# Performance work log

Hardware: AMD Instinct MI355X
Metric: run time of the kernel (lower is better)

The kernel has to match this reference:

```python
import jax, jax.numpy as jnp
import numpy as np
import math

D_MODEL = 768
D_INNER = 1536   # expand_factor=2
D_STATE = 16
DT_RANK = 48     # ceil(768/16)
D_CONV = 4
B, L = 2, 1024


def setup_inputs() -> dict:
    key = jax.random.key(0)
    ks = jax.random.split(key, 16)
    rn = lambda k, shape, s: jax.random.normal(k, shape, jnp.float32) * s
    dt_std = DT_RANK ** -0.5
    # dt bias init: softplus-inverse of dt in [dt_min, dt_max]
    dt = jnp.exp(jax.random.uniform(ks[6], (D_INNER,)) * (math.log(0.1) - math.log(0.001)) + math.log(0.001))
    dt = jnp.clip(dt, 1e-4, None)
    inv_dt = dt + jnp.log(-jnp.expm1(-dt))
    A_init = jnp.log(jnp.tile(jnp.arange(1, D_STATE + 1, dtype=jnp.float32), (D_INNER, 1)))
    return {
        "x": jax.random.normal(ks[0], (B, L, D_MODEL), jnp.float32),
        "in_proj_w": rn(ks[1], (2 * D_INNER, D_MODEL), D_MODEL ** -0.5),
        "conv_w": rn(ks[2], (D_INNER, D_CONV), D_CONV ** -0.5),
        "conv_bias": rn(ks[3], (D_INNER,), 0.02),
        "x_proj_w": rn(ks[4], (DT_RANK + 2 * D_STATE, D_INNER), D_INNER ** -0.5),
        "dt_proj_w": jax.random.uniform(ks[5], (D_INNER, DT_RANK), jnp.float32, -dt_std, dt_std),
        "dt_proj_b": inv_dt,
        "A_log": A_init,
        "D_param": jnp.ones((D_INNER,), jnp.float32),
        "out_proj_w": rn(ks[7], (D_MODEL, D_INNER), D_INNER ** -0.5),
        "A_b_log": A_init,
        "x_proj_b_w": rn(ks[8], (DT_RANK + 2 * D_STATE, D_INNER), D_INNER ** -0.5),
        "dt_proj_b_w": jax.random.uniform(ks[9], (D_INNER, DT_RANK), jnp.float32, -dt_std, dt_std),
        "dt_proj_b_b": inv_dt,
        "D_b": jnp.ones((D_INNER,), jnp.float32),
    }


def _ssm_dir(xs, A_log, Dv, xpw, dtw, dtb):
    # xs: [B, L, ED]
    A = -jnp.exp(A_log)                                  # [ED, N]
    dbc = xs @ xpw.T                                     # [B, L, dt_rank + 2N]
    delta = jax.nn.softplus(dbc[..., :DT_RANK] @ dtw.T + dtb)   # [B, L, ED]
    Bm = dbc[..., DT_RANK:DT_RANK + D_STATE]             # [B, L, N]
    Cm = dbc[..., DT_RANK + D_STATE:]                    # [B, L, N]
    dA = jnp.exp(delta[..., None] * A)                   # [B, L, ED, N]
    dBx = (delta * xs)[..., None] * Bm[:, :, None, :]    # [B, L, ED, N]

    def comb(e1, e2):
        a1, h1 = e1
        a2, h2 = e2
        return (a2 * a1, a2 * h1 + h2)

    _, hs = jax.lax.associative_scan(comb, (dA, dBx), axis=1)  # [B, L, ED, N]
    y = jnp.einsum('blen,bln->ble', hs, Cm)
    return y + Dv * xs


def reference(x, in_proj_w, conv_w, conv_bias, x_proj_w, dt_proj_w, dt_proj_b,
              A_log, D_param, out_proj_w, A_b_log, x_proj_b_w, dt_proj_b_w,
              dt_proj_b_b, D_b):
    xz = x @ in_proj_w.T                                 # [B, L, 2*ED]
    xs, z = xz[..., :D_INNER], xz[..., D_INNER:]
    # causal depthwise conv1d (torch pads both sides then slices [:L] == left pad)
    xt = jnp.transpose(xs, (0, 2, 1))                    # [B, ED, L]
    conv = jax.lax.conv_general_dilated(
        xt, conv_w[:, None, :], (1,), [(D_CONV - 1, 0)],
        feature_group_count=D_INNER,
        dimension_numbers=('NCW', 'OIW', 'NCW'))
    xs = jax.nn.silu(jnp.transpose(conv + conv_bias[:, None], (0, 2, 1)))
    y = _ssm_dir(xs, A_log, D_param, x_proj_w, dt_proj_w, dt_proj_b)
    yb = _ssm_dir(xs[:, ::-1], A_b_log, D_b, x_proj_b_w, dt_proj_b_w, dt_proj_b_b)
    y = y + yb[:, ::-1]
    return (y * jax.nn.silu(z)) @ out_proj_w.T
```

## Files before the change

kernel.cpp:

```cpp
#include <hip/hip_runtime.h>
#include <hip/hip_bf16.h>
#include <math.h>
#include <stdint.h>

#define D_MODEL 768
#define D_INNER 1536
#define D_STATE 16
#define DT_RANK 48
#define NB 2
#define LL 1024
#define MROWS (NB*LL)
#define NXZ (2*D_INNER)
#define NDBC 80

typedef __attribute__((ext_vector_type(8))) short short8;
typedef __attribute__((ext_vector_type(4))) float f32x4;

__device__ __forceinline__ float silu_f(float x) {
  return x / (1.0f + __expf(-x));
}
__device__ __forceinline__ float softplus_f(float x) {
  return (x >= 20.0f) ? x : log1pf(__expf(x));
}

__device__ __forceinline__ ushort f2bf(float x) {
  union { float f; uint32_t u; } v; v.f = x;
  return (ushort)((v.u + 0x7FFFu + ((v.u >> 16) & 1u)) >> 16);
}
__device__ __forceinline__ float bf2f(ushort h) {
  union { uint32_t u; float f; } v; v.u = ((uint32_t)h) << 16;
  return v.f;
}

__device__ __forceinline__ void g2l16(const void* g, void* l) {
  __builtin_amdgcn_global_load_lds(
      (const __attribute__((address_space(1))) uint32_t*)g,
      (__attribute__((address_space(3))) uint32_t*)l, 16, 0, 0);
}

__device__ __forceinline__ int swz(int row) {
  return (row ^ (row >> 2)) & 3;
}

__global__ __launch_bounds__(256)
void cvt_split_kernel(const float* __restrict__ in, ushort* __restrict__ hi,
                      ushort* __restrict__ lo, int n4) {
  int i = blockIdx.x * 256 + threadIdx.x;
  if (i >= n4) return;
  float4 v = *(const float4*)&in[i*4];
  ushort4 h, l;
  h.x = f2bf(v.x); l.x = f2bf(v.x - bf2f(h.x));
  h.y = f2bf(v.y); l.y = f2bf(v.y - bf2f(h.y));
  h.z = f2bf(v.z); l.z = f2bf(v.z - bf2f(h.z));
  h.w = f2bf(v.w); l.w = f2bf(v.w - bf2f(h.w));
  *(ushort4*)&hi[i*4] = h;
  *(ushort4*)&lo[i*4] = l;
}

template<int BM, int BN>
__global__ __launch_bounds__(256)
void gemm_mfma(const ushort* __restrict__ Ah, const ushort* __restrict__ Al,
               const ushort* __restrict__ Bh, const ushort* __restrict__ Bl,
               float* __restrict__ C, int M, int N, int K) {
  constexpr int MR = BM / 32;
  constexpr int NR = BN / 32;
  __shared__ __align__(16) ushort sAh[BM*32];
  __shared__ __align__(16) ushort sAl[BM*32];
  __shared__ __align__(16) ushort sBh[BN*32];
  __shared__ __align__(16) ushort sBl[BN*32];

  const int tid  = threadIdx.x;
  const int w    = tid >> 6;
  const int lane = tid & 63;
  const int wr   = w >> 1, wc = w & 1;
  const int bm   = blockIdx.x * BM, bn = blockIdx.y * BN;

  const int rA = lane >> 2;
  const int ps = lane & 3;
  const int kg = lane >> 4;
  const int fr = lane & 15;

  f32x4 acc[MR][NR];
  #pragma unroll
  for (int mi = 0; mi < MR; ++mi)
    #pragma unroll
    for (int ni = 0; ni < NR; ++ni) acc[mi][ni] = (f32x4){0.f,0.f,0.f,0.f};

  for (int k0 = 0; k0 < K; k0 += 32) {
    __syncthreads();
    #pragma unroll
    for (int q = 0; q < BM/64; ++q) {
      int row = q*64 + w*16 + rA;
      int kch = ps ^ swz(row);
      size_t go = (size_t)(bm + row)*K + k0 + kch*8;
      g2l16(Ah + go, (ushort*)sAh + (q*64 + w*16)*32);
      g2l16(Al + go, (ushort*)sAl + (q*64 + w*16)*32);
    }
    #pragma unroll
    for (int q = 0; q < BN/64; ++q) {
      int row = q*64 + w*16 + rA;
      int kch = ps ^ swz(row);
      size_t go = (size_t)(bn + row)*K + k0 + kch*8;
      g2l16(Bh + go, (ushort*)sBh + (q*64 + w*16)*32);
      g2l16(Bl + go, (ushort*)sBl + (q*64 + w*16)*32);
    }
    __syncthreads();

    short8 ah[MR], al[MR], bh[NR], bl[NR];
    #pragma unroll
    for (int mi = 0; mi < MR; ++mi) {
      int row  = wr*(BM/2) + mi*16 + fr;
      int slot = kg ^ swz(row);
      ah[mi] = *(const short8*)((const char*)sAh + row*64 + slot*16);
      al[mi] = *(const short8*)((const char*)sAl + row*64 + slot*16);
    }
    #pragma unroll
    for (int ni = 0; ni < NR; ++ni) {
      int row  = wc*(BN/2) + ni*16 + fr;
      int slot = kg ^ swz(row);
      bh[ni] = *(const short8*)((const char*)sBh + row*64 + slot*16);
      bl[ni] = *(const short8*)((const char*)sBl + row*64 + slot*16);
    }
    #pragma unroll
    for (int mi = 0; mi < MR; ++mi)
      #pragma unroll
      for (int ni = 0; ni < NR; ++ni) {
        acc[mi][ni] = __builtin_amdgcn_mfma_f32_16x16x32_bf16(ah[mi], bh[ni], acc[mi][ni], 0, 0, 0);
        acc[mi][ni] = __builtin_amdgcn_mfma_f32_16x16x32_bf16(ah[mi], bl[ni], acc[mi][ni], 0, 0, 0);
        acc[mi][ni] = __builtin_amdgcn_mfma_f32_16x16x32_bf16(al[mi], bh[ni], acc[mi][ni], 0, 0, 0);
      }
  }

  #pragma unroll
  for (int mi = 0; mi < MR; ++mi)
    #pragma unroll
    for (int ni = 0; ni < NR; ++ni) {
      #pragma unroll
      for (int r = 0; r < 4; ++r) {
        int m = bm + wr*(BM/2) + mi*16 + kg*4 + r;
        int n = bn + wc*(BN/2) + ni*16 + fr;
        C[(size_t)m*N + n] = acc[mi][ni][r];
      }
    }
}

__global__ __launch_bounds__(256)
void conv_silu_kernel(const float* __restrict__ xz, const float* __restrict__ cw,
                      const float* __restrict__ cb, float* __restrict__ xsc) {
  int idx = blockIdx.x * 256 + threadIdx.x;
  if (idx >= MROWS * D_INNER) return;
  int e   = idx % D_INNER;
  int row = idx / D_INNER;
  int l   = row % LL;
  const float* base = xz + (size_t)row * NXZ + e;
  float s = cb[e];
  #pragma unroll
  for (int j = 0; j < 4; ++j) {
    int dl = j - 3;
    if (l + dl >= 0) {
      int off = dl * NXZ;
      s = fmaf(cw[e*4 + j], base[off], s);
    }
  }
  xsc[idx] = silu_f(s);
}

__global__ __launch_bounds__(256)
void transpose_kernel(const float* __restrict__ in, float* __restrict__ outT) {
  __shared__ float T[64][65];
  const int m0 = blockIdx.x * 64;
  const int e0 = blockIdx.y * 64;
  const int cr = threadIdx.x >> 4;
  const int cc = (threadIdx.x & 15) * 4;
  for (int rr = cr; rr < 64; rr += 16) {
    float4 v = *(const float4*)&in[(size_t)(m0 + rr)*D_INNER + e0 + cc];
    T[rr][cc+0] = v.x; T[rr][cc+1] = v.y; T[rr][cc+2] = v.z; T[rr][cc+3] = v.w;
  }
  __syncthreads();
  for (int er = cr; er < 64; er += 16) {
    float4 v = make_float4(T[cc+0][er], T[cc+1][er], T[cc+2][er], T[cc+3][er]);
    *(float4*)&outT[(size_t)(e0 + er)*MROWS + m0 + cc] = v;
  }
}

__global__ __launch_bounds__(256)
void zero_kernel(float* __restrict__ p, int n) {
  int i = blockIdx.x * 256 + threadIdx.x;
  if (i < n) p[i] = 0.0f;
}

#define XP_BM 16
#define XP_KC 192
__global__ __launch_bounds__(256)
void xproj_kernel(const float* __restrict__ xsc, const float* __restrict__ wf,
                  const float* __restrict__ wb, float* __restrict__ dbcf,
                  float* __restrict__ dbcb) {
  __shared__ __align__(16) float As[16][XP_BM];
  __shared__ __align__(16) float Ws[16][164];
  const int m0    = blockIdx.x * XP_BM;
  const int kbase = blockIdx.y * XP_KC;
  const int tid = threadIdx.x;
  const int tx = tid & 31;
  const int ty = tid >> 5;
  float acc[2][5] = {};
  for (int k0 = kbase; k0 < kbase + XP_KC; k0 += 16) {
    __syncthreads();
    if (tid < 64) {
      int r = tid >> 2, c = (tid & 3) * 4;
      float4 v = *(const float4*)&xsc[(size_t)(m0 + r)*D_INNER + k0 + c];
      As[c+0][r] = v.x; As[c+1][r] = v.y; As[c+2][r] = v.z; As[c+3][r] = v.w;
    }
    for (int q = tid; q < 640; q += 256) {
      int r = q >> 2, c = (q & 3) * 4;
      const float* src = (r < 80) ? &wf[(size_t)r*D_INNER + k0 + c]
                                  : &wb[(size_t)(r-80)*D_INNER + k0 + c];
      float4 v = *(const float4*)src;
      Ws[c+0][r] = v.x; Ws[c+1][r] = v.y; Ws[c+2][r] = v.z; Ws[c+3][r] = v.w;
    }
    __syncthreads();
    #pragma unroll
    for (int kk = 0; kk < 16; ++kk) {
      float a0 = As[kk][ty*2 + 0];
      float a1 = As[kk][ty*2 + 1];
      #pragma unroll
      for (int j = 0; j < 5; ++j) {
        float w = Ws[kk][tx*5 + j];
        acc[0][j] = fmaf(a0, w, acc[0][j]);
        acc[1][j] = fmaf(a1, w, acc[1][j]);
      }
    }
  }
  #pragma unroll
  for (int i = 0; i < 2; ++i) {
    int m = m0 + ty*2 + i;
    #pragma unroll
    for (int j = 0; j < 5; ++j) {
      int n = tx*5 + j;
      float v = acc[i][j];
      if (n < 80) atomicAdd(&dbcf[(size_t)m*NDBC + n], v);
      else        atomicAdd(&dbcb[(size_t)m*NDBC + (n-80)], v);
    }
  }
}

__global__ __launch_bounds__(256)
void delta_kernel(const float* __restrict__ dbcf, const float* __restrict__ dbcb,
                  const float* __restrict__ dtwf, const float* __restrict__ dtwb,
                  const float* __restrict__ dtbf, const float* __restrict__ dtbb,
                  float* __restrict__ outf, float* __restrict__ outb) {
  const int dir = blockIdx.z;
  const float* dbc = dir ? dbcb : dbcf;
  const float* dtw = dir ? dtwb : dtwf;
  const float* dtb = dir ? dtbb : dtbf;
  float* out = dir ? outb : outf;
  __shared__ __align__(16) float As[48][36];
  __shared__ __align__(16) float Ws[48][132];
  __shared__ float T[128][33];
  const int m0 = blockIdx.x * 32;
  const int e0 = blockIdx.y * 128;
  const int tid = threadIdx.x;
  const int tx = tid & 31;
  const int ty = tid >> 5;
  for (int q = tid; q < 384; q += 256) {
    int r = q / 12, c = (q % 12) * 4;
    float4 v = *(const float4*)&dbc[(size_t)(m0 + r)*NDBC + c];
    As[c+0][r] = v.x; As[c+1][r] = v.y; As[c+2][r] = v.z; As[c+3][r] = v.w;
  }
  for (int q = tid; q < 1536; q += 256) {
    int r = q / 12, c = (q % 12) * 4;
    float4 v = *(const float4*)&dtw[(size_t)(e0 + r)*DT_RANK + c];
    Ws[c+0][r] = v.x; Ws[c+1][r] = v.y; Ws[c+2][r] = v.z; Ws[c+3][r] = v.w;
  }
  __syncthreads();
  float acc[4][4] = {};
  #pragma unroll
  for (int kk = 0; kk < 48; ++kk) {
    float4 a = *(const float4*)&As[kk][ty*4];
    float4 w = *(const float4*)&Ws[kk][tx*4];
    float av[4] = {a.x, a.y, a.z, a.w};
    float wv[4] = {w.x, w.y, w.z, w.w};
    #pragma unroll
    for (int i = 0; i < 4; ++i)
      #pragma unroll
      for (int j = 0; j < 4; ++j)
        acc[i][j] = fmaf(av[i], wv[j], acc[i][j]);
  }
  #pragma unroll
  for (int i = 0; i < 4; ++i)
    #pragma unroll
    for (int j = 0; j < 4; ++j)
      T[tx*4 + j][ty*4 + i] = softplus_f(acc[i][j] + dtb[e0 + tx*4 + j]);
  __syncthreads();
  {
    int r = tid >> 1, h = (tid & 1) * 16;
    float* dst = out + (size_t)(e0 + r)*MROWS + m0 + h;
    #pragma unroll
    for (int q = 0; q < 4; ++q) {
      float4 v = make_float4(T[r][h+q*4+0], T[r][h+q*4+1], T[r][h+q*4+2], T[r][h+q*4+3]);
      *(float4*)(dst + q*4) = v;
    }
  }
}

#define SC_C 16
#define SC_P 64
__global__ __launch_bounds__(1024)
void scan_kernel(const float* __restrict__ dltf, const float* __restrict__ dltb,
                 const float* __restrict__ dbcf, const float* __restrict__ dbcb,
                 const float* __restrict__ xst,
                 const float* __restrict__ Alogf, const float* __restrict__ Alogb,
                 float* __restrict__ yf, float* __restrict__ yb) {
  __shared__ float sA[SC_C][4][16];
  __shared__ float sH[SC_C][4][16];
  __shared__ float sI[SC_C][4][16];
  const int blk = blockIdx.x;
  const int dir = blk / 768;
  const int b   = (blk % 768) / 384;
  const int e0  = (blk % 384) * 4;
  const int tid = threadIdx.x;
  const int c   = tid >> 6;
  const int lane = tid & 63;
  const int es  = lane >> 4;
  const int n   = lane & 15;
  const int e   = e0 + es;

  const float* dlt  = dir ? dltb  : dltf;
  const float* dbc  = dir ? dbcb  : dbcf;
  const float* Alog = dir ? Alogb : Alogf;
  float* y          = dir ? yb    : yf;

  const float a2 = -__expf(Alog[e*D_STATE + n]) * 1.4426950408889634f;

  const int sg = dir ? -1 : 1;
  const int l0 = dir ? (LL - 1 - c*SC_P) : (c*SC_P);

  const float* dp0 = dlt + (size_t)e * MROWS + b * LL + l0;
  const float* xp0 = xst + (size_t)e * MROWS + b * LL + l0;
  const float* bp0 = dbc + ((size_t)b * LL + l0) * NDBC + DT_RANK + n;

  {
    const float* d = dp0;
    const float* x = xp0;
    const float* bc = bp0;
    float Ap = 1.0f, hh = 0.0f;
    #pragma unroll 8
    for (int i = 0; i < SC_P; ++i) {
      const float dl = *d;
      const float xv = *x;
      const float Bv = *bc;
      const float dA = exp2f(dl * a2);
      hh = fmaf(dA, hh, dl * xv * Bv);
      Ap *= dA;
      d += sg; x += sg; bc += sg * NDBC;
    }
    sA[c][es][n] = Ap;
    sH[c][es][n] = hh;
  }
  __syncthreads();

  if (tid < 64) {
    float carry = 0.0f;
    #pragma unroll
    for (int cc = 0; cc < SC_C; ++cc) {
      sI[cc][es][n] = carry;
      carry = fmaf(sA[cc][es][n], carry, sH[cc][es][n]);
    }
  }
  __syncthreads();

  {
    const float* d = dp0;
    const float* x = xp0;
    const float* bc = bp0;
    float* yw = y + (size_t)b * LL * D_INNER + e + (size_t)l0 * D_INNER;
    const int ystep = sg * D_INNER;
    float h = sI[c][es][n];
    #pragma unroll 8
    for (int i = 0; i < SC_P; ++i) {
      const float dl = *d;
      const float xv = *x;
      const float Bv = *bc;
      const float Cv = bc[D_STATE];
      const float dA = exp2f(dl * a2);
      h = fmaf(dA, h, dl * xv * Bv);
      float p = h * Cv;
      p += __shfl_xor(p, 1);
      p += __shfl_xor(p, 2);
      p += __shfl_xor(p, 4);
      p += __shfl_xor(p, 8);
      if (n == 0) *yw = p;
      d += sg; x += sg; bc += sg * NDBC; yw += ystep;
    }
  }
}

__global__ __launch_bounds__(256)
void gate_kernel(const float* __restrict__ yf, const float* __restrict__ yb,
                 const float* __restrict__ xsc, const float* __restrict__ xz,
                 const float* __restrict__ Dp, const float* __restrict__ Db,
                 ushort* __restrict__ ghi, ushort* __restrict__ glo) {
  int i4 = blockIdx.x * 256 + threadIdx.x;
  if (i4 >= MROWS * D_INNER / 4) return;
  int idx = i4 * 4;
  int e   = idx % D_INNER;
  int row = idx / D_INNER;
  float4 vf = *(const float4*)&yf[idx];
  float4 vb = *(const float4*)&yb[idx];
  float4 vx = *(const float4*)&xsc[idx];
  float4 vz = *(const float4*)&xz[(size_t)row*NXZ + D_INNER + e];
  float4 vD  = *(const float4*)&Dp[e];
  float4 vDb = *(const float4*)&Db[e];
  float4 o;
  o.x = fmaf(vD.x + vDb.x, vx.x, vf.x + vb.x) * silu_f(vz.x);
  o.y = fmaf(vD.y + vDb.y, vx.y, vf.y + vb.y) * silu_f(vz.y);
  o.z = fmaf(vD.z + vDb.z, vx.z, vf.z + vb.z) * silu_f(vz.z);
  o.w = fmaf(vD.w + vDb.w, vx.w, vf.w + vb.w) * silu_f(vz.w);
  ushort4 h, l;
  h.x = f2bf(o.x); l.x = f2bf(o.x - bf2f(h.x));
  h.y = f2bf(o.y); l.y = f2bf(o.y - bf2f(h.y));
  h.z = f2bf(o.z); l.z = f2bf(o.z - bf2f(h.z));
  h.w = f2bf(o.w); l.w = f2bf(o.w - bf2f(h.w));
  *(ushort4*)&ghi[idx] = h;
  *(ushort4*)&glo[idx] = l;
}

extern "C" void kernel_launch(void* const* d_in, const int* in_sizes, int n_in,
                              void* d_out, int out_size, void* d_ws, size_t ws_size,
                              hipStream_t stream) {
  const float* x     = (const float*)d_in[0];
  const float* ipw   = (const float*)d_in[1];
  const float* cw    = (const float*)d_in[2];
  const float* cb    = (const float*)d_in[3];
  const float* xpwf  = (const float*)d_in[4];
  const float* dtwf  = (const float*)d_in[5];
  const float* dtbf  = (const float*)d_in[6];
  const float* Alogf = (const float*)d_in[7];
  const float* Dpf   = (const float*)d_in[8];
  const float* opw   = (const float*)d_in[9];
  const float* Alogb = (const float*)d_in[10];
  const float* xpwb  = (const float*)d_in[11];
  const float* dtwb  = (const float*)d_in[12];
  const float* dtbb  = (const float*)d_in[13];
  const float* Dpb   = (const float*)d_in[14];
  float* out = (float*)d_out;

  float* ws = (float*)d_ws;
  float* xz   = ws;
  float* xsc  = xz   + (size_t)MROWS * NXZ;
  float* dbcf = xsc  + (size_t)MROWS * D_INNER;
  float* dbcb = dbcf + (size_t)MROWS * NDBC;
  float* dltf = dbcb + (size_t)MROWS * NDBC;
  float* dltb = dltf + (size_t)MROWS * D_INNER;
  float* yfb  = dltb + (size_t)MROWS * D_INNER;
  float* ybb  = yfb  + (size_t)MROWS * D_INNER;
  ushort* xhi   = (ushort*)yfb;
  ushort* xlo   = xhi   + (size_t)MROWS * D_MODEL;
  ushort* ipwhi = (ushort*)ybb;
  ushort* ipwlo = ipwhi + (size_t)NXZ * D_MODEL;
  ushort* opwhi = (ushort*)(ybb + (size_t)MROWS * D_INNER);
  ushort* opwlo = opwhi + (size_t)D_MODEL * D_INNER;
  float*  xst   = (float*)(opwlo + (size_t)D_MODEL * D_INNER);
  ushort* ghi = (ushort*)dltf;
  ushort* glo = ghi + (size_t)MROWS * D_INNER;

  cvt_split_kernel<<<dim3(MROWS*D_MODEL/4/256), 256, 0, stream>>>(x, xhi, xlo, MROWS*D_MODEL/4);
  cvt_split_kernel<<<dim3(NXZ*D_MODEL/4/256), 256, 0, stream>>>(ipw, ipwhi, ipwlo, NXZ*D_MODEL/4);
  cvt_split_kernel<<<dim3(D_MODEL*D_INNER/4/256), 256, 0, stream>>>(opw, opwhi, opwlo, D_MODEL*D_INNER/4);

  gemm_mfma<128,128><<<dim3(MROWS/128, NXZ/128), 256, 0, stream>>>(
      xhi, xlo, ipwhi, ipwlo, xz, MROWS, NXZ, D_MODEL);
  conv_silu_kernel<<<dim3((MROWS*D_INNER)/256), 256, 0, stream>>>(xz, cw, cb, xsc);
  transpose_kernel<<<dim3(MROWS/64, D_INNER/64), 256, 0, stream>>>(xsc, xst);
  zero_kernel<<<dim3((MROWS*2*NDBC + 255)/256), 256, 0, stream>>>(dbcf, MROWS*2*NDBC);
  xproj_kernel<<<dim3(MROWS/XP_BM, D_INNER/XP_KC), 256, 0, stream>>>(
      xsc, xpwf, xpwb, dbcf, dbcb);
  delta_kernel<<<dim3(MROWS/32, D_INNER/128, 2), 256, 0, stream>>>(
      dbcf, dbcb, dtwf, dtwb, dtbf, dtbb, dltf, dltb);
  scan_kernel<<<dim3(1536), 1024, 0, stream>>>(
      dltf, dltb, dbcf, dbcb, xst, Alogf, Alogb, yfb, ybb);
  gate_kernel<<<dim3((MROWS*D_INNER/4)/256), 256, 0, stream>>>(
      yfb, ybb, xsc, xz, Dpf, Dpb, ghi, glo);
  gemm_mfma<64,64><<<dim3(MROWS/64, D_MODEL/64), 256, 0, stream>>>(
      ghi, glo, opwhi, opwlo, out, MROWS, D_MODEL, D_INNER);
}
```

Measured before the change: 474.8 us.

## Give each scan thread four SSM states and sixteen channels per block

The selective-scan kernel now assigns four state indices per thread instead of one. Each wavefront covers 16 channels rather than 4, and the grid shrinks from 1536 to 384 blocks. Per-timestep delta and x loads are now shared across four states, B and C are read as float4, and the shuffle reduction drops from four steps to two. In exchange there are fewer blocks to fill the GPU, more registers per thread, and more serial exp2 work per thread.

```diff
diff --git a/kernel.cpp b/kernel.cpp
--- a/kernel.cpp
+++ b/kernel.cpp
@@ -310,86 +310,100 @@
                  const float* __restrict__ xst,
                  const float* __restrict__ Alogf, const float* __restrict__ Alogb,
                  float* __restrict__ yf, float* __restrict__ yb) {
-  __shared__ float sA[SC_C][4][16];
-  __shared__ float sH[SC_C][4][16];
-  __shared__ float sI[SC_C][4][16];
+  __shared__ float sA[SC_C][16][16];
+  __shared__ float sH[SC_C][16][16];
+  __shared__ float sI[SC_C][16][16];
   const int blk = blockIdx.x;
-  const int dir = blk / 768;
-  const int b   = (blk % 768) / 384;
-  const int e0  = (blk % 384) * 4;
+  const int dir = blk / 192;
+  const int b   = (blk % 192) / 96;
+  const int e0  = (blk % 96) * 16;
   const int tid = threadIdx.x;
   const int c   = tid >> 6;
   const int lane = tid & 63;
-  const int es  = lane >> 4;
-  const int n   = lane & 15;
-  const int e   = e0 + es;
+  const int el  = lane >> 2;
+  const int q   = lane & 3;
+  const int e   = e0 + el;
 
   const float* dlt  = dir ? dltb  : dltf;
   const float* dbc  = dir ? dbcb  : dbcf;
   const float* Alog = dir ? Alogb : Alogf;
   float* y          = dir ? yb    : yf;
 
-  const float a2 = -__expf(Alog[e*D_STATE + n]) * 1.4426950408889634f;
+  const float LOG2E = 1.4426950408889634f;
+  float4 av = *(const float4*)&Alog[e*D_STATE + q*4];
+  float a2[4] = { -__expf(av.x)*LOG2E, -__expf(av.y)*LOG2E,
+                  -__expf(av.z)*LOG2E, -__expf(av.w)*LOG2E };
 
   const int sg = dir ? -1 : 1;
   const int l0 = dir ? (LL - 1 - c*SC_P) : (c*SC_P);
 
   const float* dp0 = dlt + (size_t)e * MROWS + b * LL + l0;
   const float* xp0 = xst + (size_t)e * MROWS + b * LL + l0;
-  const float* bp0 = dbc + ((size_t)b * LL + l0) * NDBC + DT_RANK + n;
-
+  const float* bp0 = dbc + ((size_t)b * LL + l0) * NDBC + DT_RANK + q*4;
+  const int bstep = sg * NDBC;
+
+  float Ap[4] = {1.f,1.f,1.f,1.f}, hh[4] = {0.f,0.f,0.f,0.f};
   {
-    const float* d = dp0;
-    const float* x = xp0;
-    const float* bc = bp0;
-    float Ap = 1.0f, hh = 0.0f;
-    #pragma unroll 8
+    const float* d = dp0; const float* x = xp0; const float* bc = bp0;
+    #pragma unroll 4
     for (int i = 0; i < SC_P; ++i) {
-      const float dl = *d;
-      const float xv = *x;
-      const float Bv = *bc;
-      const float dA = exp2f(dl * a2);
-      hh = fmaf(dA, hh, dl * xv * Bv);
-      Ap *= dA;
-      d += sg; x += sg; bc += sg * NDBC;
-    }
-    sA[c][es][n] = Ap;
-    sH[c][es][n] = hh;
+      const float dl = *d, xv = *x;
+      const float4 B = *(const float4*)bc;
+      const float u = dl * xv;
+      const float Bv[4] = {B.x, B.y, B.z, B.w};
+      #pragma unroll
+      for (int j = 0; j < 4; ++j) {
+        const float dA = exp2f(dl * a2[j]);
+        hh[j] = fmaf(dA, hh[j], u * Bv[j]);
+        Ap[j] *= dA;
+      }
+      d += sg; x += sg; bc += bstep;
+    }
+  }
+  #pragma unroll
+  for (int j = 0; j < 4; ++j) {
+    sA[c][el][q*4+j] = Ap[j];
+    sH[c][el][q*4+j] = hh[j];
   }
   __syncthreads();
 
-  if (tid < 64) {
+  if (tid < 256) {
+    const int ee = tid >> 4, nn = tid & 15;
     float carry = 0.0f;
     #pragma unroll
     for (int cc = 0; cc < SC_C; ++cc) {
-      sI[cc][es][n] = carry;
-      carry = fmaf(sA[cc][es][n], carry, sH[cc][es][n]);
+      sI[cc][ee][nn] = carry;
+      carry = fmaf(sA[cc][ee][nn], carry, sH[cc][ee][nn]);
     }
   }
   __syncthreads();
 
+  float h[4];
+  #pragma unroll
+  for (int j = 0; j < 4; ++j) h[j] = sI[c][el][q*4+j];
   {
-    const float* d = dp0;
-    const float* x = xp0;
-    const float* bc = bp0;
+    const float* d = dp0; const float* x = xp0; const float* bc = bp0;
     float* yw = y + (size_t)b * LL * D_INNER + e + (size_t)l0 * D_INNER;
-    const int ystep = sg * D_INNER;
-    float h = sI[c][es][n];
-    #pragma unroll 8
+    const int ystep = sg * (int)D_INNER;
+    #pragma unroll 4
     for (int i = 0; i < SC_P; ++i) {
-      const float dl = *d;
-      const float xv = *x;
-      const float Bv = *bc;
-      const float Cv = bc[D_STATE];
-      const float dA = exp2f(dl * a2);
-      h = fmaf(dA, h, dl * xv * Bv);
-      float p = h * Cv;
+      const float dl = *d, xv = *x;
+      const float4 B = *(const float4*)bc;
+      const float4 C = *(const float4*)(bc + D_STATE);
+      const float u = dl * xv;
+      const float Bv[4] = {B.x, B.y, B.z, B.w};
+      const float Cv[4] = {C.x, C.y, C.z, C.w};
+      float p = 0.0f;
+      #pragma unroll
+      for (int j = 0; j < 4; ++j) {
+        const float dA = exp2f(dl * a2[j]);
+        h[j] = fmaf(dA, h[j], u * Bv[j]);
+        p = fmaf(h[j], Cv[j], p);
+      }
       p += __shfl_xor(p, 1);
       p += __shfl_xor(p, 2);
-      p += __shfl_xor(p, 4);
-      p += __shfl_xor(p, 8);
-      if (n == 0) *yw = p;
-      d += sg; x += sg; bc += sg * NDBC; yw += ystep;
+      if (q == 0) *yw = p;
+      d += sg; x += sg; bc += bstep; yw += ystep;
     }
   }
 }
@@ -476,7 +490,7 @@
       xsc, xpwf, xpwb, dbcf, dbcb);
   delta_kernel<<<dim3(MROWS/32, D_INNER/128, 2), 256, 0, stream>>>(
       dbcf, dbcb, dtwf, dtwb, dtbf, dtbb, dltf, dltb);
-  scan_kernel<<<dim3(1536), 1024, 0, stream>>>(
+  scan_kernel<<<dim3(384), 1024, 0, stream>>>(
       dltf, dltb, dbcf, dbcb, xst, Alogf, Alogb, yfb, ybb);
   gate_kernel<<<dim3((MROWS*D_INNER/4)/256), 256, 0, stream>>>(
       yfb, ybb, xsc, xz, Dpf, Dpb, ghi, glo);
```

Result: slower. 514.8 us (+8.4%).
